# Kernel optimization log

Measured on AMD Instinct MI355X. Metric: run time of the kernel, lower is better.

Reference implementation:

```python
import jax, jax.numpy as jnp
import numpy as np

DN = ('NCHW', 'OIHW', 'NCHW')
WINDOW_SIZES = (11, 25, 49)


def conv(x, w, b=None, pad=0, groups=1):
    y = jax.lax.conv_general_dilated(
        x, w, window_strides=(1, 1), padding=((pad, pad), (pad, pad)),
        dimension_numbers=DN, feature_group_count=groups)
    if b is not None:
        y = y + b[None, :, None, None]
    return y


def box_mean(f, wsize):
    # depthwise box-filter local mean with reflect padding (matches F.pad mode='reflect')
    C = f.shape[1]
    p = wsize // 2
    fp = jnp.pad(f, ((0, 0), (0, 0), (p, p), (p, p)), mode='reflect')
    k = jnp.ones((C, 1, wsize, wsize), f.dtype) / (wsize * wsize)
    return conv(fp, k, groups=C)


def std_map(features, wsize):
    # per-channel local std, channel-weighted sum, then **0.8
    C = features.shape[1]
    # C == 8 here, so weights are softmax(ones) == uniform (torch path for C != 4)
    cw = jax.nn.softmax(jnp.ones((C,), features.dtype))
    m = box_mean(features, wsize)
    m2 = box_mean(features ** 2, wsize)
    var = jnp.clip(m2 - m ** 2, 1e-6, None)
    res = jnp.sum(cw[None, :, None, None] * jnp.sqrt(var), axis=1, keepdims=True)
    return res ** 0.8  # [B,1,H,W]


def setup_inputs() -> dict:
    key = jax.random.key(0)
    ks = jax.random.split(key, 8)
    B, C, H, W = 8, 4, 512, 512
    x = jax.random.normal(ks[0], (B, C, H, W), dtype=jnp.float32)
    conv1_w = jax.random.normal(ks[1], (32, 4, 3, 3), dtype=jnp.float32) * 0.1
    conv1_b = jnp.zeros((32,), jnp.float32)
    conv2_w = jax.random.normal(ks[2], (16, 32, 3, 3), dtype=jnp.float32) * 0.05
    conv2_b = jnp.zeros((16,), jnp.float32)
    conv3_w = jax.random.normal(ks[3], (8, 16, 3, 3), dtype=jnp.float32) * 0.05
    conv3_b = jnp.zeros((8,), jnp.float32)
    # scale_fusion init: weight = 1/len(window_sizes), bias = 0
    fusion_w = jnp.full((1, len(WINDOW_SIZES), 1, 1), 1.0 / len(WINDOW_SIZES), jnp.float32)
    fusion_b = jnp.zeros((1,), jnp.float32)
    channel_weights = jnp.ones((4,), jnp.float32) / 4.0
    return dict(x=x, conv1_w=conv1_w, conv1_b=conv1_b, conv2_w=conv2_w,
                conv2_b=conv2_b, conv3_w=conv3_w, conv3_b=conv3_b,
                fusion_w=fusion_w, fusion_b=fusion_b,
                channel_weights=channel_weights)


def reference(x, conv1_w, conv1_b, conv2_w, conv2_b, conv3_w, conv3_b,
              fusion_w, fusion_b, channel_weights):
    lrelu = lambda v: jnp.where(v >= 0, v, 0.2 * v)
    # feature extractor: conv3x3 -> lrelu -> conv3x3 -> lrelu -> conv3x3
    f = lrelu(conv(x, conv1_w, conv1_b, pad=1))
    f = lrelu(conv(f, conv2_w, conv2_b, pad=1))
    f = conv(f, conv3_w, conv3_b, pad=1)  # [B,8,H,W]
    # multi-scale std maps
    maps = [std_map(f, w) for w in WINDOW_SIZES]
    multi = jnp.concatenate(maps, axis=1)  # [B,3,H,W]
    fused = jax.nn.relu(conv(multi, fusion_w, fusion_b, pad=0))  # [B,1,H,W]
    # adaptive thresholds (global quantiles over the whole fused std map)
    qs = jnp.quantile(fused.reshape(-1), jnp.array([0.25, 0.75], fused.dtype))
    q25, q75 = qs[0], qs[1]
    iqr = q75 - q25
    gstd = jnp.std(x, axis=(2, 3), keepdims=True, ddof=1)  # [B,4,1,1] (torch unbiased)
    lo = (q25 - 0.5 * iqr) * jnp.ones_like(gstd)
    hi = (q75 + 0.5 * iqr) * jnp.ones_like(gstd)
    gf = jnp.clip(gstd * 5.0, 0.5, 2.0)
    lo, hi = lo * gf, hi * gf
    cw = jax.nn.softmax(channel_weights)[None, :, None, None]
    cstd = jnp.std(x * cw, axis=(2, 3), keepdims=True, ddof=1)
    cf = jnp.clip(cstd * 2.0, 0.8, 1.2)
    lo, hi = lo * cf, hi * cf
    # mask generation: broadcast [B,1,H,W] vs [B,4,1,1] -> [B,4,H,W], then mean over C
    n = jnp.clip((fused - lo) / (hi - lo), 0.0, 1.0)
    mask = jax.nn.sigmoid(6.0 * n - 3.0)
    return jnp.mean(mask, axis=1, keepdims=True)  # [B,1,H,W]
```

## Files before the change

### kernel.cpp

```cpp
#include <hip/hip_runtime.h>
#include <cmath>

#define HH 512
#define WW 512
#define NB 8
#define CIN 4
#define C2 32
#define C3 16
#define CF 8
#define HW (HH*WW)
#define NPIX (NB*HW)
#define NBC 2

#define SEGC 10
#define SW   320
#define SVW  ((SW + (SW>>4) + 3) | 1)
#define RSW  (256 + 16 + 2)

__device__ __forceinline__ float lrelu_f(float v){ return v < 0.f ? 0.2f*v : v; }
__device__ __forceinline__ int reflect_i(int i){ int r = i < 0 ? -i : i; return r >= HH ? 2*HH - 2 - r : r; }
__device__ __forceinline__ int swz(int j){ return j + (j >> 4); }

template<int Ci, int Co, bool LRELU>
__global__ __launch_bounds__(256) void k_conv8(const float* __restrict__ in,
                                               const float* __restrict__ wgt,
                                               const float* __restrict__ bias,
                                               float* __restrict__ outp)
{
    constexpr int NG = Co/8;
    __shared__ float wl[NG*Ci*72];
    __shared__ float bl[Co];
    for (int i = threadIdx.x; i < Co*Ci*9; i += 256){
        int g  = i / (Ci*72);
        int r  = i - g*(Ci*72);
        int ci = r / 72;
        int q  = r - ci*72;
        int tap = q >> 3, ocl = q & 7;
        wl[i] = wgt[((g*8 + ocl)*Ci + ci)*9 + tap];
    }
    if (threadIdx.x < Co) bl[threadIdx.x] = bias[threadIdx.x];
    __syncthreads();

    int bid   = blockIdx.x;
    int local = bid % (NG*128);
    int b     = bid / (NG*128);
    int cb    = local & 3;
    int rb    = (local >> 2) & 31;
    int cg    = local >> 7;
    int tid   = threadIdx.x;
    int lane  = tid & 31;
    int col   = cb*128 + lane*4;
    int row0  = rb*16  + (tid >> 5)*2;
    int co0   = cg*8;
    const float* inb = in + (size_t)b*Ci*HW;

    float acc[8][2][4];
    #pragma unroll
    for (int j=0;j<8;j++){
        float bv = bl[co0+j];
        #pragma unroll
        for (int r=0;r<2;r++)
            #pragma unroll
            for (int p=0;p<4;p++) acc[j][r][p] = bv;
    }

    #pragma unroll 1
    for (int ci=0; ci<Ci; ci++){
        float v[4][6];
        const float* inc = inb + (size_t)ci*HW;
        #pragma unroll
        for (int dy=0;dy<4;dy++){
            int hh = row0 + dy - 1;
            int hc = hh < 0 ? 0 : (hh > HH-1 ? HH-1 : hh);
            bool hok = (unsigned)hh < (unsigned)HH;
            const float* rowp = inc + hc*WW;
            float4 m  = *(const float4*)(rowp + col);
            float  v0 = (col > 0)      ? rowp[col-1] : 0.f;
            float  v5 = (col+4 < WW)   ? rowp[col+4] : 0.f;
            if (!hok){ m.x=0.f; m.y=0.f; m.z=0.f; m.w=0.f; v0=0.f; v5=0.f; }
            v[dy][0]=v0; v[dy][1]=m.x; v[dy][2]=m.y;
            v[dy][3]=m.z; v[dy][4]=m.w; v[dy][5]=v5;
        }
        const float* wp = &wl[(cg*Ci + ci)*72];
        #pragma unroll
        for (int t=0;t<9;t++){
            int dy = t/3, dx = t - 3*(t/3);
            float w8[8];
            #pragma unroll
            for (int o=0;o<8;o++) w8[o] = wp[t*8 + o];
            #pragma unroll
            for (int o=0;o<8;o++)
                #pragma unroll
                for (int r=0;r<2;r++)
                    #pragma unroll
                    for (int p=0;p<4;p++)
                        acc[o][r][p] = fmaf(v[dy+r][dx+p], w8[o], acc[o][r][p]);
        }
    }

    float* ob = outp + (size_t)b*Co*HW;
    #pragma unroll
    for (int j=0;j<8;j++){
        #pragma unroll
        for (int r=0;r<2;r++){
            float4 o;
            o.x = LRELU ? lrelu_f(acc[j][r][0]) : acc[j][r][0];
            o.y = LRELU ? lrelu_f(acc[j][r][1]) : acc[j][r][1];
            o.z = LRELU ? lrelu_f(acc[j][r][2]) : acc[j][r][2];
            o.w = LRELU ? lrelu_f(acc[j][r][3]) : acc[j][r][3];
            *(float4*)(ob + (size_t)(co0+j)*HW + (size_t)(row0+r)*WW + col) = o;
        }
    }
}

template<int WS>
__device__ __forceinline__ float scale_step(float2* __restrict__ svq,
                                            float* __restrict__ resv,
                                            const float* vs, const float* vq,
                                            float fws)
{
    constexpr int P   = WS/2;
    constexpr int OFF = 24 - P;
    constexpr float inv = 1.f/((float)WS*(float)WS);
    const int tid = threadIdx.x;
    const int ch  = tid >> 5;
    const int seg = tid & 31;

    __syncthreads();
    #pragma unroll
    for (int k=0;k<SEGC;k++){
        int j = k*32 + seg;
        svq[ch*SVW + swz(j)] = make_float2(vs[k], vq[k]);
    }
    __syncthreads();

    int base = OFF + seg*8;
    float S = 0.f, Q = 0.f;
    #pragma unroll
    for (int q=0;q<WS;q++){
        float2 t = svq[ch*SVW + swz(base+q)];
        S += t.x; Q += t.y;
    }
    float res[8];
    #pragma unroll
    for (int t8=0;t8<8;t8++){
        float m = S*inv, m2 = Q*inv;
        res[t8] = sqrtf(fmaxf(fmaf(-m, m, m2), 1e-6f));
        if (t8 < 7){
            float2 ta = svq[ch*SVW + swz(base+t8+WS)];
            float2 tb = svq[ch*SVW + swz(base+t8)];
            S += ta.x - tb.x; Q += ta.y - tb.y;
        }
    }
    #pragma unroll
    for (int t8=0;t8<8;t8++)
        resv[ch*RSW + swz(seg*8+t8)] = res[t8];
    __syncthreads();

    float a = 0.f;
    #pragma unroll
    for (int cc=0;cc<CF;cc++) a += resv[cc*RSW + swz(tid)];
    return fws * powf(a*0.125f, 0.8f);
}

__global__ __launch_bounds__(256) void k_std3(const float* __restrict__ f,
                                              float* __restrict__ fused,
                                              const float* __restrict__ fwv)
{
    __shared__ float2 svq[CF*SVW];
    __shared__ float  resv[CF*RSW];

    int bid  = blockIdx.x;
    int band = bid & 31;
    int half = (bid >> 5) & 1;
    int b    = bid >> 6;
    int r0   = band*16;
    int c0   = half*256;
    int tid  = threadIdx.x;
    int ch   = tid >> 5;
    int seg  = tid & 31;
    const float* fp = f + (size_t)(b*CF + ch)*HW;

    int rc[SEGC];
    #pragma unroll
    for (int k=0;k<SEGC;k++){
        int gc = c0 - 24 + k*32 + seg;
        gc = gc < 0 ? -gc : (gc > WW-1 ? 2*WW-2 - gc : gc);
        rc[k] = gc;
    }

    float vs49[SEGC], vq49[SEGC], vs25[SEGC], vq25[SEGC], vs11[SEGC], vq11[SEGC];
    #pragma unroll
    for (int k=0;k<SEGC;k++){
        vs49[k]=0.f; vq49[k]=0.f; vs25[k]=0.f; vq25[k]=0.f; vs11[k]=0.f; vq11[k]=0.f;
    }
    #pragma unroll 1
    for (int dy=-24; dy<=24; dy++){
        const float* rp = fp + (size_t)reflect_i(r0+dy)*WW;
        bool in25 = (dy >= -12 && dy <= 12);
        bool in11 = (dy >= -5  && dy <= 5);
        #pragma unroll
        for (int k=0;k<SEGC;k++){
            float v = rp[rc[k]]; float v2 = v*v;
            vs49[k] += v; vq49[k] += v2;
            if (in25){ vs25[k] += v; vq25[k] += v2; }
            if (in11){ vs11[k] += v; vq11[k] += v2; }
        }
    }

    float fw0 = fwv[0], fw1 = fwv[1], fw2 = fwv[2];

    for (int rr=0; rr<16; rr++){
        int r = r0 + rr;
        float val;
        val  = scale_step<11>(svq, resv, vs11, vq11, fw0);
        val += scale_step<25>(svq, resv, vs25, vq25, fw1);
        val += scale_step<49>(svq, resv, vs49, vq49, fw2);
        fused[((size_t)b*HH + r)*WW + c0 + tid] = val;
        if (rr < 15){
            {   const float* ep = fp + (size_t)reflect_i(r+25)*WW;
                const float* lp = fp + (size_t)reflect_i(r-24)*WW;
                #pragma unroll
                for (int k=0;k<SEGC;k++){
                    float e = ep[rc[k]], l = lp[rc[k]];
                    vs49[k] += e - l;
                    vq49[k] = fmaf(e, e, vq49[k]); vq49[k] = fmaf(-l, l, vq49[k]);
                }
            }
            {   const float* ep = fp + (size_t)reflect_i(r+13)*WW;
                const float* lp = fp + (size_t)reflect_i(r-12)*WW;
                #pragma unroll
                for (int k=0;k<SEGC;k++){
                    float e = ep[rc[k]], l = lp[rc[k]];
                    vs25[k] += e - l;
                    vq25[k] = fmaf(e, e, vq25[k]); vq25[k] = fmaf(-l, l, vq25[k]);
                }
            }
            {   const float* ep = fp + (size_t)reflect_i(r+6)*WW;
                const float* lp = fp + (size_t)reflect_i(r-5)*WW;
                #pragma unroll
                for (int k=0;k<SEGC;k++){
                    float e = ep[rc[k]], l = lp[rc[k]];
                    vs11[k] += e - l;
                    vq11[k] = fmaf(e, e, vq11[k]); vq11[k] = fmaf(-l, l, vq11[k]);
                }
            }
        }
    }
}

__global__ void k_h8(const float* __restrict__ fused, const float* __restrict__ fb,
                     unsigned* __restrict__ hist8)
{
    __shared__ unsigned lh[256];
    lh[threadIdx.x] = 0;
    __syncthreads();
    float fbv = fb[0];
    int i = blockIdx.x*256 + threadIdx.x;
    int stride = gridDim.x*256;
    for (; i < NPIX; i += stride){
        float v = fmaxf(fused[i] + fbv, 0.f);
        atomicAdd(&lh[__float_as_uint(v) >> 24], 1u);
    }
    __syncthreads();
    if (lh[threadIdx.x]) atomicAdd(&hist8[threadIdx.x], lh[threadIdx.x]);
}

__global__ void k_scan8(const unsigned* __restrict__ hist8,
                        int* __restrict__ cand8, int* __restrict__ rank8)
{
    if (threadIdx.x == 0){
        const unsigned RK[4] = {524287u, 524288u, 1572863u, 1572864u};
        unsigned cum = 0; int qi = 0;
        for (int b = 0; b < 256 && qi < 4; b++){
            unsigned cnt = hist8[b];
            while (qi < 4 && RK[qi] < cum + cnt){
                cand8[qi] = b; rank8[qi] = (int)(RK[qi] - cum); qi++;
            }
            cum += cnt;
        }
    }
}

__global__ void k_h8b(const float* __restrict__ fused, const float* __restrict__ fb,
                      const int* __restrict__ cand8, unsigned* __restrict__ hist8b)
{
    __shared__ unsigned lh[1024];
    for (int i = threadIdx.x; i < 1024; i += 256) lh[i] = 0;
    __syncthreads();
    float fbv = fb[0];
    int c0 = cand8[0], c1 = cand8[1], c2 = cand8[2], c3 = cand8[3];
    bool d1 = (c1 != c0);
    bool d2 = (c2 != c0) && (c2 != c1);
    bool d3 = (c3 != c0) && (c3 != c1) && (c3 != c2);
    int i = blockIdx.x*256 + threadIdx.x;
    int stride = gridDim.x*256;
    for (; i < NPIX; i += stride){
        unsigned u = __float_as_uint(fmaxf(fused[i] + fbv, 0.f));
        int hi = (int)(u >> 24);
        unsigned mid = (u >> 16) & 0xffu;
        if (hi == c0)       atomicAdd(&lh[mid],       1u);
        if (d1 && hi == c1) atomicAdd(&lh[256u+mid],  1u);
        if (d2 && hi == c2) atomicAdd(&lh[512u+mid],  1u);
        if (d3 && hi == c3) atomicAdd(&lh[768u+mid],  1u);
    }
    __syncthreads();
    for (int i = threadIdx.x; i < 1024; i += 256)
        if (lh[i]) atomicAdd(&hist8b[i], lh[i]);
}

__global__ void k_scan8b(const unsigned* __restrict__ hist8b,
                         const int* __restrict__ cand8, const int* __restrict__ rank8,
                         int* __restrict__ cand16, int* __restrict__ rank16)
{
    int qi = threadIdx.x;
    if (qi < 4){
        int slot = qi;
        for (int j = 0; j < qi; j++) if (cand8[j] == cand8[qi]){ slot = j; break; }
        const unsigned* h = hist8b + slot*256;
        unsigned k = (unsigned)rank8[qi], cum = 0;
        for (int b = 0; b < 256; b++){
            unsigned cnt = h[b];
            if (cnt && k >= cum && k < cum + cnt){
                cand16[qi] = (cand8[qi] << 8) | b;
                rank16[qi] = (int)(k - cum);
            }
            cum += cnt;
        }
    }
}

__global__ void k_h16(const float* __restrict__ fused, const float* __restrict__ fb,
                      const int* __restrict__ cand16, unsigned* __restrict__ histlo)
{
    float fbv = fb[0];
    int c0 = cand16[0], c1 = cand16[1], c2 = cand16[2], c3 = cand16[3];
    bool d1 = (c1 != c0);
    bool d2 = (c2 != c0) && (c2 != c1);
    bool d3 = (c3 != c0) && (c3 != c1) && (c3 != c2);
    int i = blockIdx.x*256 + threadIdx.x;
    int stride = gridDim.x*256;
    for (; i < NPIX; i += stride){
        unsigned u = __float_as_uint(fmaxf(fused[i] + fbv, 0.f));
        int hi = (int)(u >> 16);
        unsigned lo = u & 0xffffu;
        if (hi == c0)       atomicAdd(&histlo[lo],           1u);
        if (d1 && hi == c1) atomicAdd(&histlo[65536u + lo],  1u);
        if (d2 && hi == c2) atomicAdd(&histlo[131072u + lo], 1u);
        if (d3 && hi == c3) atomicAdd(&histlo[196608u + lo], 1u);
    }
}

__global__ void k_scan16(const unsigned* __restrict__ histlo,
                         const int* __restrict__ cand16, const int* __restrict__ rank16,
                         float* __restrict__ ostat)
{
    int qi = blockIdx.x;
    int slot = qi;
    for (int j = 0; j < qi; j++) if (cand16[j] == cand16[qi]){ slot = j; break; }
    const unsigned* hist = histlo + (size_t)slot*65536;
    __shared__ unsigned csum[256];
    __shared__ unsigned cbase[256];
    int t = threadIdx.x;
    unsigned s = 0;
    for (int i = 0; i < 256; i++) s += hist[t*256 + i];
    csum[t] = s;
    __syncthreads();
    if (t == 0){ unsigned run = 0; for (int i = 0; i < 256; i++){ cbase[i] = run; run += csum[i]; } }
    __syncthreads();
    unsigned k = (unsigned)rank16[qi];
    unsigned cum = cbase[t];
    for (int i = 0; i < 256; i++){
        unsigned cnt = hist[t*256 + i];
        if (cnt && k >= cum && k < cum + cnt)
            ostat[qi] = __uint_as_float(((unsigned)cand16[qi] << 16) | (unsigned)(t*256 + i));
        cum += cnt;
    }
}

__global__ void k_gstd_part(const float* __restrict__ x, double* __restrict__ part)
{
    int bid = blockIdx.x;
    int plane = bid >> 3, chunk = bid & 7;
    const float4* p4 = (const float4*)(x + (size_t)plane*HW + (size_t)chunk*32768);
    int t = threadIdx.x;
    double s=0.0, s2=0.0;
    for (int k=0;k<32;k++){
        float4 v = p4[k*256 + t];
        s  += (double)v.x + (double)v.y + (double)v.z + (double)v.w;
        s2 += (double)v.x*v.x + (double)v.y*v.y + (double)v.z*v.z + (double)v.w*v.w;
    }
    __shared__ double rs[256], rq[256];
    rs[t]=s; rq[t]=s2; __syncthreads();
    for (int off=128; off>0; off>>=1){
        if (t<off){ rs[t]+=rs[t+off]; rq[t]+=rq[t+off]; }
        __syncthreads();
    }
    if (t==0){ part[bid*2]=rs[0]; part[bid*2+1]=rq[0]; }
}

__global__ void k_gstd_final(const double* __restrict__ part, float* __restrict__ gstd)
{
    int t = threadIdx.x;
    if (t < 32){
        double s=0.0, s2=0.0;
        for (int j=0;j<8;j++){ s += part[(t*8+j)*2]; s2 += part[(t*8+j)*2+1]; }
        const double N = 262144.0;
        double var = (s2 - s*s/N) / (N - 1.0);
        gstd[t] = (float)sqrt(var < 0.0 ? 0.0 : var);
    }
}

__global__ void k_finalize(const float* __restrict__ ostat, const float* __restrict__ gstd,
                           const float* __restrict__ cwin, float* __restrict__ lov, float* __restrict__ hiv)
{
    int t = threadIdx.x;
    if (t < 32){
        float q25 = ostat[0] + 0.75f*(ostat[1]-ostat[0]);
        float q75 = ostat[2] + 0.25f*(ostat[3]-ostat[2]);
        float iqr = q75 - q25;
        float lo_b = q25 - 0.5f*iqr, hi_b = q75 + 0.5f*iqr;
        int c = t & 3;
        float m = fmaxf(fmaxf(cwin[0],cwin[1]), fmaxf(cwin[2],cwin[3]));
        float e0 = expf(cwin[0]-m), e1 = expf(cwin[1]-m), e2 = expf(cwin[2]-m), e3 = expf(cwin[3]-m);
        float smc = expf(cwin[c]-m) / (e0+e1+e2+e3);
        float g  = gstd[t];
        float gf = fminf(fmaxf(g*5.f, 0.5f), 2.f);
        float cf = fminf(fmaxf(smc*g*2.f, 0.8f), 1.2f);
        lov[t] = lo_b*gf*cf;
        hiv[t] = hi_b*gf*cf;
    }
}

__global__ void k_mask(const float* __restrict__ fused_in, const float* __restrict__ fb,
                       const float* __restrict__ lov, const float* __restrict__ hiv,
                       float* __restrict__ outp)
{
    int i = blockIdx.x*256 + threadIdx.x;
    float F = fmaxf(fused_in[i] + fb[0], 0.f);
    int b = i >> 18;
    float o = 0.f;
    #pragma unroll
    for (int c=0;c<4;c++){
        float lo = lov[b*4+c], hi = hiv[b*4+c];
        float n = (F - lo) / (hi - lo);
        n = fminf(fmaxf(n, 0.f), 1.f);
        o += 1.f/(1.f + expf(3.f - 6.f*n));
    }
    outp[i] = 0.25f * o;
}

extern "C" void kernel_launch(void* const* d_in, const int* in_sizes, int n_in,
                              void* d_out, int out_size, void* d_ws, size_t ws_size,
                              hipStream_t stream)
{
    const float* x  = (const float*)d_in[0];
    const float* w1 = (const float*)d_in[1];
    const float* b1 = (const float*)d_in[2];
    const float* w2 = (const float*)d_in[3];
    const float* b2 = (const float*)d_in[4];
    const float* w3 = (const float*)d_in[5];
    const float* b3 = (const float*)d_in[6];
    const float* fw = (const float*)d_in[7];
    const float* fb = (const float*)d_in[8];
    const float* cw = (const float*)d_in[9];
    float* out = (float*)d_out;
    char* ws = (char*)d_ws;

    size_t off = 0;
    auto take = [&](size_t bytes)->size_t{ size_t o = off; off += (bytes + 255) & ~(size_t)255; return o; };
    size_t o_h8     = take(256*4);
    size_t o_h8b    = take(1024*4);
    size_t o_histlo = take((size_t)4*65536*4);
    size_t o_c8     = take(4*4);
    size_t o_r8     = take(4*4);
    size_t o_c16    = take(4*4);
    size_t o_r16    = take(4*4);
    size_t o_os     = take(4*4);
    size_t o_part   = take(512*8);
    size_t o_gs     = take(32*4);
    size_t o_lo     = take(32*4);
    size_t o_hi     = take(32*4);
    size_t o_R1     = take((size_t)NB*C3*HW*4);
    size_t o_R2     = take((size_t)NBC*C2*HW*4);

    float*    f2buf  = (float*)(ws + o_R1);
    float*    f1     = (float*)(ws + o_R2);
    float*    fbuf   = (float*)(ws + o_R2);
    unsigned* hist8  = (unsigned*)(ws + o_h8);
    unsigned* hist8b = (unsigned*)(ws + o_h8b);
    unsigned* histlo = (unsigned*)(ws + o_histlo);
    int*      c8     = (int*)(ws + o_c8);
    int*      r8     = (int*)(ws + o_r8);
    int*      c16    = (int*)(ws + o_c16);
    int*      r16    = (int*)(ws + o_r16);
    float*    osv    = (float*)(ws + o_os);
    double*   part   = (double*)(ws + o_part);
    float*    gs     = (float*)(ws + o_gs);
    float*    lov    = (float*)(ws + o_lo);
    float*    hiv    = (float*)(ws + o_hi);
    size_t hist_bytes = (o_histlo + (size_t)4*65536*4) - o_h8;

    for (int ck = 0; ck < NB/NBC; ck++){
        const float* xb = x + (size_t)ck*NBC*CIN*HW;
        k_conv8<CIN,C2,true ><<<NBC*512,256,0,stream>>>(xb, w1, b1, f1);
        k_conv8<C2, C3,true ><<<NBC*256,256,0,stream>>>(f1, w2, b2,
                                                        f2buf + (size_t)ck*NBC*C3*HW);
    }
    k_conv8<C3, CF, false><<<NB*128,256,0,stream>>>(f2buf, w3, b3, fbuf);

    k_gstd_part<<<256,256,0,stream>>>(x, part);
    k_gstd_final<<<1,256,0,stream>>>(part, gs);

    k_std3<<<NB*2*32,256,0,stream>>>(fbuf, out, fw);

    hipMemsetAsync(hist8, 0, hist_bytes, stream);
    k_h8    <<<2048,256,0,stream>>>(out, fb, hist8);
    k_scan8 <<<1,64,0,stream>>>(hist8, c8, r8);
    k_h8b   <<<2048,256,0,stream>>>(out, fb, c8, hist8b);
    k_scan8b<<<1,64,0,stream>>>(hist8b, c8, r8, c16, r16);
    k_h16   <<<2048,256,0,stream>>>(out, fb, c16, histlo);
    k_scan16<<<4,256,0,stream>>>(histlo, c16, r16, osv);

    k_finalize<<<1,64,0,stream>>>(osv, gs, cw, lov, hiv);
    k_mask<<<NPIX/256,256,0,stream>>>(out, fb, lov, hiv, out);
}
```

Measured before the change: 827.4 us.

## Software-prefetch next input channel in conv kernels and widen LDS swizzle padding

Adds a PF template flag to the 3x3 conv kernel that loads the next input channel's rows into registers while the current channel's FMAs run, so global-load latency overlaps compute in conv1 and conv2. Row offsets and bounds flags are hoisted out of the channel loop. Separately, the shared-memory swizzle in the std kernels changes from one pad per 16 elements to one per 8, with wider row strides. The prefetch raises register pressure, which could lower occupancy, and the larger LDS footprint may also reduce occupancy.

Result: slower. 930.9 us (+12.5%).

```diff
diff --git a/kernel.cpp b/kernel.cpp
--- a/kernel.cpp
+++ b/kernel.cpp
@@ -14,14 +14,14 @@
 
 #define SEGC 10
 #define SW   320
-#define SVW  ((SW + (SW>>4) + 3) | 1)
-#define RSW  (256 + 16 + 2)
+#define SVW  ((SW + (SW>>3) + 4) | 1)
+#define RSW  (256 + 32 + 4)
 
 __device__ __forceinline__ float lrelu_f(float v){ return v < 0.f ? 0.2f*v : v; }
 __device__ __forceinline__ int reflect_i(int i){ int r = i < 0 ? -i : i; return r >= HH ? 2*HH - 2 - r : r; }
-__device__ __forceinline__ int swz(int j){ return j + (j >> 4); }
-
-template<int Ci, int Co, bool LRELU>
+__device__ __forceinline__ int swz(int j){ return j + (j >> 3); }
+
+template<int Ci, int Co, bool LRELU, bool PF>
 __global__ __launch_bounds__(256) void k_conv8(const float* __restrict__ in,
                                                const float* __restrict__ wgt,
                                                const float* __restrict__ bias,
@@ -54,6 +54,15 @@
     int co0   = cg*8;
     const float* inb = in + (size_t)b*Ci*HW;
 
+    int  hcofs[4]; bool hok[4];
+    #pragma unroll
+    for (int dy=0;dy<4;dy++){
+        int hh = row0 + dy - 1;
+        int hc = hh < 0 ? 0 : (hh > HH-1 ? HH-1 : hh);
+        hok[dy]   = (unsigned)hh < (unsigned)HH;
+        hcofs[dy] = hc*WW;
+    }
+
     float acc[8][2][4];
     #pragma unroll
     for (int j=0;j<8;j++){
@@ -64,22 +73,50 @@
             for (int p=0;p<4;p++) acc[j][r][p] = bv;
     }
 
+    float4 m[4]; float ea[4], eb[4];
+    if constexpr (PF){
+        #pragma unroll
+        for (int dy=0;dy<4;dy++){
+            const float* rowp = inb + hcofs[dy];
+            m[dy]  = *(const float4*)(rowp + col);
+            ea[dy] = (col > 0)    ? rowp[col-1] : 0.f;
+            eb[dy] = (col+4 < WW) ? rowp[col+4] : 0.f;
+        }
+    }
+
     #pragma unroll 1
     for (int ci=0; ci<Ci; ci++){
+        if constexpr (!PF){
+            const float* inc = inb + (size_t)ci*HW;
+            #pragma unroll
+            for (int dy=0;dy<4;dy++){
+                const float* rowp = inc + hcofs[dy];
+                m[dy]  = *(const float4*)(rowp + col);
+                ea[dy] = (col > 0)    ? rowp[col-1] : 0.f;
+                eb[dy] = (col+4 < WW) ? rowp[col+4] : 0.f;
+            }
+        }
+        float4 mn[4]; float ean[4], ebn[4];
+        if constexpr (PF){
+            if (ci+1 < Ci){
+                const float* inc = inb + (size_t)(ci+1)*HW;
+                #pragma unroll
+                for (int dy=0;dy<4;dy++){
+                    const float* rowp = inc + hcofs[dy];
+                    mn[dy]  = *(const float4*)(rowp + col);
+                    ean[dy] = (col > 0)    ? rowp[col-1] : 0.f;
+                    ebn[dy] = (col+4 < WW) ? rowp[col+4] : 0.f;
+                }
+            }
+        }
+
         float v[4][6];
-        const float* inc = inb + (size_t)ci*HW;
         #pragma unroll
         for (int dy=0;dy<4;dy++){
-            int hh = row0 + dy - 1;
-            int hc = hh < 0 ? 0 : (hh > HH-1 ? HH-1 : hh);
-            bool hok = (unsigned)hh < (unsigned)HH;
-            const float* rowp = inc + hc*WW;
-            float4 m  = *(const float4*)(rowp + col);
-            float  v0 = (col > 0)      ? rowp[col-1] : 0.f;
-            float  v5 = (col+4 < WW)   ? rowp[col+4] : 0.f;
-            if (!hok){ m.x=0.f; m.y=0.f; m.z=0.f; m.w=0.f; v0=0.f; v5=0.f; }
-            v[dy][0]=v0; v[dy][1]=m.x; v[dy][2]=m.y;
-            v[dy][3]=m.z; v[dy][4]=m.w; v[dy][5]=v5;
+            float4 mm = m[dy]; float v0 = ea[dy], v5 = eb[dy];
+            if (!hok[dy]){ mm.x=0.f; mm.y=0.f; mm.z=0.f; mm.w=0.f; v0=0.f; v5=0.f; }
+            v[dy][0]=v0; v[dy][1]=mm.x; v[dy][2]=mm.y;
+            v[dy][3]=mm.z; v[dy][4]=mm.w; v[dy][5]=v5;
         }
         const float* wp = &wl[(cg*Ci + ci)*72];
         #pragma unroll
@@ -95,6 +132,12 @@
                     #pragma unroll
                     for (int p=0;p<4;p++)
                         acc[o][r][p] = fmaf(v[dy+r][dx+p], w8[o], acc[o][r][p]);
+        }
+        if constexpr (PF){
+            if (ci+1 < Ci){
+                #pragma unroll
+                for (int dy=0;dy<4;dy++){ m[dy]=mn[dy]; ea[dy]=ean[dy]; eb[dy]=ebn[dy]; }
+            }
         }
     }
 
@@ -503,11 +546,11 @@
 
     for (int ck = 0; ck < NB/NBC; ck++){
         const float* xb = x + (size_t)ck*NBC*CIN*HW;
-        k_conv8<CIN,C2,true ><<<NBC*512,256,0,stream>>>(xb, w1, b1, f1);
-        k_conv8<C2, C3,true ><<<NBC*256,256,0,stream>>>(f1, w2, b2,
+        k_conv8<CIN,C2,true ,true ><<<NBC*512,256,0,stream>>>(xb, w1, b1, f1);
+        k_conv8<C2, C3,true ,true ><<<NBC*256,256,0,stream>>>(f1, w2, b2,
                                                         f2buf + (size_t)ck*NBC*C3*HW);
     }
-    k_conv8<C3, CF, false><<<NB*128,256,0,stream>>>(f2buf, w3, b3, fbuf);
+    k_conv8<C3, CF, false,false><<<NB*128,256,0,stream>>>(f2buf, w3, b3, fbuf);
 
     k_gstd_part<<<256,256,0,stream>>>(x, part);
     k_gstd_final<<<1,256,0,stream>>>(part, gs);
```
